# Optimization experiments

Measured on AMD Instinct MI355X. Metric: run time of the kernel, lower is better.

Reference implementation:

```python
import jax, jax.numpy as jnp
import numpy as np

WINDOW_SIZE = 11  # 2*h_patch_size + 1 with h_patch_size=5
SIGMA = 1.5
C1 = 0.01 ** 2
C2 = 0.03 ** 2


def _window2d():
    x = np.arange(WINDOW_SIZE) - WINDOW_SIZE // 2
    g = np.exp(-(x ** 2) / (2.0 * SIGMA ** 2))
    g = g / g.sum()
    w = np.outer(g, g)  # [ws, ws], sums to 1
    return jnp.asarray(w, dtype=jnp.float32)


def setup_inputs() -> dict:
    key = jax.random.key(0)
    k1, k2 = jax.random.split(key)
    n_view, N, n_p, npatch, C = 4, 2048, 16, 121, 3
    img_pred = jax.random.uniform(k1, (n_view, N, n_p, npatch, C), dtype=jnp.float32)
    img_gt = jax.random.uniform(k2, (N, n_p, npatch, C), dtype=jnp.float32)
    return {"img_pred": img_pred, "img_gt": img_gt}


def reference(img_pred, img_gt):
    # img_pred: [n_view, N, n_p, npatch, C]; img_gt: [N, n_p, npatch, C]
    n_view, N, n_p, npatch, C = img_pred.shape
    ps = WINDOW_SIZE  # patch_size == window_size since conv has padding=0 and output is 1x1
    w = _window2d()  # [ps, ps]

    pred = img_pred.reshape(n_view, N, n_p, ps, ps, C)
    gt = img_gt.reshape(1, N, n_p, ps, ps, C)

    # Depthwise 11x11 conv on an 11x11 patch with padding=0 == gaussian-weighted sum.
    def wsum(x):
        return jnp.einsum('vnphwc,hw->vnpc', x, w)

    mu1 = wsum(pred)                      # [n_view, N, n_p, C]
    mu2 = wsum(gt)                        # [1, N, n_p, C]
    mu1_sq = mu1 * mu1
    mu2_sq = mu2 * mu2
    mu1_mu2 = mu1 * mu2
    sigma1_sq = wsum(pred * pred) - mu1_sq
    sigma2_sq = wsum(gt * gt) - mu2_sq    # [1, N, n_p, C]
    sigma12 = wsum(pred * gt) - mu1_mu2   # pred*gt broadcasts over n_view

    ssim_map = ((2.0 * mu1_mu2 + C1) * (2.0 * sigma12 + C2)) / (
        (mu1_sq + mu2_sq + C1) * (sigma1_sq + sigma2_sq + C2))
    return ssim_map.mean(-1)  # [n_view, N, n_p]
```

## Files before the change

### kernel.cpp

```cpp
#include <hip/hip_runtime.h>


static constexpr int N_OUT   = 4 * 2048 * 16;
static constexpr int NP_MASK = 2048 * 16 - 1;
static constexpr int OPB     = 16;
static constexpr int FLT_BLK = OPB * 363;
static constexpr int VEC_BLK = FLT_BLK / 4;

__device__ __constant__ float G11[11] = {
    0.00102838f, 0.00759875f, 0.03600077f, 0.10936070f, 0.21300555f,
    0.26601173f,
    0.21300555f, 0.10936070f, 0.03600077f, 0.00759875f, 0.00102838f
};

__device__ __forceinline__ float red16(float v) {
    v += __shfl_xor(v, 1);
    v += __shfl_xor(v, 2);
    v += __shfl_xor(v, 4);
    v += __shfl_xor(v, 8);
    return v;
}

__global__ __launch_bounds__(256, 4) void ssim_kernel(
    const float* __restrict__ pred, const float* __restrict__ gt,
    float* __restrict__ out)
{
    __shared__ float4 predS4[VEC_BLK];
    __shared__ float  W[128];

    const int t     = threadIdx.x;
    const int lane  = t & 15;
    const int group = t >> 4;
    const int o     = blockIdx.x * OPB + group;

    const float* g = gt + (size_t)(o & NP_MASK) * 363;
    float gv[8][3];
    #pragma unroll
    for (int rnd = 0; rnd < 8; ++rnd) {
        const int pix = lane + rnd * 16;
        const int pc  = (pix < 121 ? pix : 120) * 3;
        gv[rnd][0] = g[pc];
        gv[rnd][1] = g[pc + 1];
        gv[rnd][2] = g[pc + 2];
    }

    if (t < 128) {
        float w = 0.f;
        if (t < 121) {
            const int r = t / 11;
            const int c = t - r * 11;
            w = G11[r] * G11[c];
        }
        W[t] = w;
    }

    const float4* p4 = (const float4*)(pred + (size_t)blockIdx.x * FLT_BLK);
    #pragma unroll
    for (int r = 0; r < 6; ++r) {
        const int idx = t + r * 256;
        if (idx < VEC_BLK) predS4[idx] = p4[idx];
    }
    __syncthreads();

    const float* p = (const float*)predS4 + group * 363;

    float mu1[3] = {0.f, 0.f, 0.f};
    float mu2[3] = {0.f, 0.f, 0.f};
    float s1 [3] = {0.f, 0.f, 0.f};
    float s2 [3] = {0.f, 0.f, 0.f};
    float s12[3] = {0.f, 0.f, 0.f};

    #pragma unroll
    for (int rnd = 0; rnd < 8; ++rnd) {
        const int pix = lane + rnd * 16;
        const float w = W[pix];
        const int pc  = (pix < 121 ? pix : 120) * 3;
        const float pv[3] = {p[pc], p[pc + 1], p[pc + 2]};
        #pragma unroll
        for (int c = 0; c < 3; ++c) {
            const float pvc = pv[c];
            const float gvc = gv[rnd][c];
            const float tp = w * pvc;
            const float tg = w * gvc;
            mu1[c] += tp;
            mu2[c] += tg;
            s1 [c] = fmaf(tp, pvc, s1 [c]);
            s2 [c] = fmaf(tg, gvc, s2 [c]);
            s12[c] = fmaf(tp, gvc, s12[c]);
        }
    }

    #pragma unroll
    for (int c = 0; c < 3; ++c) {
        mu1[c] = red16(mu1[c]);
        mu2[c] = red16(mu2[c]);
        s1 [c] = red16(s1 [c]);
        s2 [c] = red16(s2 [c]);
        s12[c] = red16(s12[c]);
    }

    if (lane == 0) {
        const float C1 = 1e-4f;
        const float C2 = 9e-4f;
        float acc = 0.f;
        #pragma unroll
        for (int c = 0; c < 3; ++c) {
            const float m1 = mu1[c], m2 = mu2[c];
            const float m1sq = m1 * m1, m2sq = m2 * m2, m12 = m1 * m2;
            const float sig1 = s1[c]  - m1sq;
            const float sig2 = s2[c]  - m2sq;
            const float sg12 = s12[c] - m12;
            const float num = (2.f * m12 + C1) * (2.f * sg12 + C2);
            const float den = (m1sq + m2sq + C1) * (sig1 + sig2 + C2);
            acc += num / den;
        }
        out[o] = acc * (1.f / 3.f);
    }
}

extern "C" void kernel_launch(void* const* d_in, const int* in_sizes, int n_in,
                              void* d_out, int out_size, void* d_ws, size_t ws_size,
                              hipStream_t stream) {
    const float* pred = (const float*)d_in[0];
    const float* gt   = (const float*)d_in[1];
    float* out        = (float*)d_out;
    ssim_kernel<<<N_OUT / OPB, 256, 0, stream>>>(pred, gt, out);
}
```

Measured before the change: 292.1 us.

## Share gt patch loads across all four views within each block

Each block now handles 4 spatial patches across all 4 views, staging the gt chunk into shared memory once and reusing it for every view. Before, each view's block reread gt from global memory with per-thread scalar loads. The change cuts gt traffic and turns gt loads into coalesced float4 copies. The cost is four strided pred chunk loads per block, one per view.

```diff
diff --git a/kernel.cpp b/kernel.cpp
--- a/kernel.cpp
+++ b/kernel.cpp
@@ -1,11 +1,11 @@
 #include <hip/hip_runtime.h>
 
 
-static constexpr int N_OUT   = 4 * 2048 * 16;
-static constexpr int NP_MASK = 2048 * 16 - 1;
-static constexpr int OPB     = 16;
-static constexpr int FLT_BLK = OPB * 363;
-static constexpr int VEC_BLK = FLT_BLK / 4;
+static constexpr int NPATCH         = 2048 * 16;
+static constexpr int PPB            = 4;
+static constexpr int NBLK           = NPATCH / PPB;
+static constexpr int CHUNK_F4       = PPB * 363 / 4;
+static constexpr int VIEW_STRIDE_F4 = NPATCH * 363 / 4;
 
 __device__ __constant__ float G11[11] = {
     0.00102838f, 0.00759875f, 0.03600077f, 0.10936070f, 0.21300555f,
@@ -25,23 +25,24 @@
     const float* __restrict__ pred, const float* __restrict__ gt,
     float* __restrict__ out)
 {
-    __shared__ float4 predS4[VEC_BLK];
+    __shared__ float4 predS4[4 * CHUNK_F4];
+    __shared__ float4 gtS4[CHUNK_F4];
     __shared__ float  W[128];
 
-    const int t     = threadIdx.x;
-    const int lane  = t & 15;
-    const int group = t >> 4;
-    const int o     = blockIdx.x * OPB + group;
+    const int t = threadIdx.x;
+    const int b = blockIdx.x;
 
-    const float* g = gt + (size_t)(o & NP_MASK) * 363;
-    float gv[8][3];
+    const float4* gsrc = (const float4*)gt + (size_t)b * CHUNK_F4;
+    gtS4[t] = gsrc[t];
+    if (t < CHUNK_F4 - 256) gtS4[t + 256] = gsrc[t + 256];
+
+    const float4* psrc0 = (const float4*)pred + (size_t)b * CHUNK_F4;
     #pragma unroll
-    for (int rnd = 0; rnd < 8; ++rnd) {
-        const int pix = lane + rnd * 16;
-        const int pc  = (pix < 121 ? pix : 120) * 3;
-        gv[rnd][0] = g[pc];
-        gv[rnd][1] = g[pc + 1];
-        gv[rnd][2] = g[pc + 2];
+    for (int v = 0; v < 4; ++v) {
+        const float4* src = psrc0 + (size_t)v * VIEW_STRIDE_F4;
+        float4* dst = predS4 + v * CHUNK_F4;
+        dst[t] = src[t];
+        if (t < CHUNK_F4 - 256) dst[t + 256] = src[t + 256];
     }
 
     if (t < 128) {
@@ -53,16 +54,15 @@
         }
         W[t] = w;
     }
-
-    const float4* p4 = (const float4*)(pred + (size_t)blockIdx.x * FLT_BLK);
-    #pragma unroll
-    for (int r = 0; r < 6; ++r) {
-        const int idx = t + r * 256;
-        if (idx < VEC_BLK) predS4[idx] = p4[idx];
-    }
     __syncthreads();
 
-    const float* p = (const float*)predS4 + group * 363;
+    const int lane = t & 15;
+    const int grp  = t >> 4;
+    const int v    = grp >> 2;
+    const int s    = grp & 3;
+
+    const float* p = (const float*)predS4 + (v * PPB + s) * 363;
+    const float* g = (const float*)gtS4 + s * 363;
 
     float mu1[3] = {0.f, 0.f, 0.f};
     float mu2[3] = {0.f, 0.f, 0.f};
@@ -76,10 +76,11 @@
         const float w = W[pix];
         const int pc  = (pix < 121 ? pix : 120) * 3;
         const float pv[3] = {p[pc], p[pc + 1], p[pc + 2]};
+        const float gv[3] = {g[pc], g[pc + 1], g[pc + 2]};
         #pragma unroll
         for (int c = 0; c < 3; ++c) {
             const float pvc = pv[c];
-            const float gvc = gv[rnd][c];
+            const float gvc = gv[c];
             const float tp = w * pvc;
             const float tg = w * gvc;
             mu1[c] += tp;
@@ -114,7 +115,7 @@
             const float den = (m1sq + m2sq + C1) * (sig1 + sig2 + C2);
             acc += num / den;
         }
-        out[o] = acc * (1.f / 3.f);
+        out[v * NPATCH + b * PPB + s] = acc * (1.f / 3.f);
     }
 }
 
@@ -124,5 +125,5 @@
     const float* pred = (const float*)d_in[0];
     const float* gt   = (const float*)d_in[1];
     float* out        = (float*)d_out;
-    ssim_kernel<<<N_OUT / OPB, 256, 0, stream>>>(pred, gt, out);
+    ssim_kernel<<<NBLK, 256, 0, stream>>>(pred, gt, out);
 }
```

New measurement: 293.0 us. No clear change (+0.3%).
